# Performance work log

Measured on AMD Instinct MI355X. Metric: run time of the kernel, lower is better.

The kernel has to match this reference:

```python
import jax, jax.numpy as jnp
import numpy as np

D, H, DH, DF = 128, 8, 16, 512
N_Q, N_KV, E = 20000, 20000, 640000


def _xavier(key, shape):
    fan_in, fan_out = shape[1], shape[0]
    lim = float(np.sqrt(6.0 / (fan_in + fan_out)))
    return jax.random.uniform(key, shape, jnp.float32, -lim, lim)


def layer_norm(x, g, b, eps=1e-5):
    mu = jnp.mean(x, axis=-1, keepdims=True)
    var = jnp.var(x, axis=-1, keepdims=True)
    return (x - mu) * jax.lax.rsqrt(var + eps) * g + b


def setup_inputs() -> dict:
    key = jax.random.key(0)
    ks = jax.random.split(key, 12)
    return {
        "q_feat": jax.random.normal(ks[0], (N_Q, D), jnp.float32),
        "kv_feat": jax.random.normal(ks[1], (N_KV, D), jnp.float32),
        "src": jax.random.randint(ks[2], (E,), 0, N_KV, jnp.int32),
        "dst": jax.random.randint(ks[3], (E,), 0, N_Q, jnp.int32),
        "Wq": _xavier(ks[4], (H * DH, D)),
        "Wk": _xavier(ks[5], (H * DH, D)),
        "Wv": _xavier(ks[6], (H * DH, D)),
        "Wo": _xavier(ks[7], (D, H * DH)),
        "W1": _xavier(ks[8], (DF, D)),
        "bf1": jnp.zeros((DF,), jnp.float32),
        "W2": _xavier(ks[9], (D, DF)),
        "bf2": jnp.zeros((D,), jnp.float32),
        "ln1_g": jnp.ones((D,), jnp.float32),
        "ln1_b": jnp.zeros((D,), jnp.float32),
        "ln2_g": jnp.ones((D,), jnp.float32),
        "ln2_b": jnp.zeros((D,), jnp.float32),
    }


def reference(q_feat, kv_feat, src, dst, Wq, Wk, Wv, Wo, W1, bf1, W2, bf2,
              ln1_g, ln1_b, ln2_g, ln2_b):
    n_q = q_feat.shape[0]
    # projections -> [N, H, DH]
    q = (q_feat @ Wq.T).reshape(-1, H, DH)
    k = (kv_feat @ Wk.T).reshape(-1, H, DH)
    v = (kv_feat @ Wv.T).reshape(-1, H, DH)
    # edge scores: u_mul_v then sum over d_head, scaled (score per edge per head)
    score = jnp.einsum('ehd,ehd->eh', k[src], q[dst]) / np.sqrt(DH)
    # edge_softmax grouped by destination node
    mx = jax.ops.segment_max(score, dst, num_segments=n_q)  # [Nq, H]
    ex = jnp.exp(score - mx[dst])
    denom = jax.ops.segment_sum(ex, dst, num_segments=n_q)
    att = ex / denom[dst]  # [E, H]
    # weighted scatter-sum of values to destination nodes
    msg = v[src] * att[:, :, None]  # [E, H, DH]
    out = jax.ops.segment_sum(msg, dst, num_segments=n_q)  # [Nq, H, DH]
    sa = out.reshape(n_q, H * DH) @ Wo.T
    feat = layer_norm(q_feat + sa, ln1_g, ln1_b)
    ff = jax.nn.relu(feat @ W1.T + bf1) @ W2.T + bf2
    return layer_norm(feat + ff, ln2_g, ln2_b)
```

## Files before the change

### kernel.cpp

```cpp
#include <hip/hip_runtime.h>
#include <hip/hip_fp16.h>
#include <math.h>
#include <type_traits>

#define D 128
#define NH 8
#define DHD 16
#define DF 512
#define STR 128
#define NSH 8
#define SSL 64

typedef _Float16 half8 __attribute__((ext_vector_type(8)));
typedef _Float16 half4 __attribute__((ext_vector_type(4)));
typedef float f32x4 __attribute__((ext_vector_type(4)));


__global__ __launch_bounds__(256) void mega_kernel(
    const float* __restrict__ q_feat, const float* __restrict__ kv_feat,
    const float* __restrict__ Wq, const float* __restrict__ Wk,
    const float* __restrict__ Wv,
    __half* __restrict__ fq, __half* __restrict__ fkv, int NQ, int NKV,
    const int* __restrict__ dst, const int* __restrict__ src,
    int* __restrict__ cnt, unsigned short* __restrict__ srcg, int E,
    const float* __restrict__ Wo, const float* __restrict__ W1,
    const float* __restrict__ W2,
    __half* __restrict__ wo16, __half* __restrict__ w116, __half* __restrict__ w216) {
    __shared__ __align__(16) __half As[64 * 128];
    __shared__ __align__(16) __half Ws[64 * 128];

    int xt = blockIdx.x;
    int tid = threadIdx.x;

    if (xt >= 2) {
        if (xt == (int)gridDim.x - 1) {
            int g = blockIdx.y * 256 + tid;
            if (g < 36864) {
                const float* s;
                __half* d;
                int idx = g;
                if (idx < 4096) { s = Wo; d = wo16; }
                else if (idx < 20480) { idx -= 4096; s = W1; d = w116; }
                else { idx -= 20480; s = W2; d = w216; }
                float4 f = ((const float4*)s)[idx];
                ushort4 o;
                o.x = __half_as_ushort(__float2half(f.x));
                o.y = __half_as_ushort(__float2half(f.y));
                o.z = __half_as_ushort(__float2half(f.z));
                o.w = __half_as_ushort(__float2half(f.w));
                ((ushort4*)d)[idx] = o;
            }
            return;
        }
        int b = (xt - 2) * gridDim.y + blockIdx.y;
        int sh = (blockIdx.x + blockIdx.y * gridDim.x) & (NSH - 1);
        int i4 = b * 256 + tid;
        int base = i4 << 2;
        if (base < E) {
            if (base + 3 < E) {
                int4 d4 = ((const int4*)dst)[i4];
                int4 s4 = ((const int4*)src)[i4];
                int dd[4] = {d4.x, d4.y, d4.z, d4.w};
                int ss[4] = {s4.x, s4.y, s4.z, s4.w};
#pragma unroll
                for (int u = 0; u < 4; ++u) {
                    int p = atomicAdd(&cnt[dd[u] * NSH + sh], 1);
                    if (p < SSL)
                        srcg[((size_t)dd[u] << 9) + (sh << 6) + p] = (unsigned short)ss[u];
                }
            } else {
                for (int u = 0; u < 4 && base + u < E; ++u) {
                    int dn = dst[base + u];
                    int sn = src[base + u];
                    int p = atomicAdd(&cnt[dn * NSH + sh], 1);
                    if (p < SSL)
                        srcg[((size_t)dn << 9) + (sh << 6) + p] = (unsigned short)sn;
                }
            }
        }
        return;
    }

    const float* A = xt ? kv_feat : q_feat;
    __half* C = xt ? fkv : fq;
    int O = xt ? 256 : 128;
    int NCT = xt ? 4 : 2;
    int N = xt ? NKV : NQ;
    int row0 = blockIdx.y * 64;
    if (row0 >= N) return;

    int lane = tid & 63;
    int w = tid >> 6;
    int l16 = lane & 15, lq = lane >> 4;

#pragma unroll
    for (int i = 0; i < 4; ++i) {
        int f = tid + i * 256;
        int ln = f & 63;
        int mt = (f >> 6) & 3;
        int kc = f >> 8;
        int m = row0 + mt * 16 + (ln & 15);
        int k = kc * 32 + (ln >> 4) * 8;
        half8 v = {};
        if (m < N) {
            const float4* p = (const float4*)(A + (size_t)m * 128 + k);
            float4 f0 = p[0], f1 = p[1];
            v = (half8){(_Float16)f0.x, (_Float16)f0.y, (_Float16)f0.z, (_Float16)f0.w,
                        (_Float16)f1.x, (_Float16)f1.y, (_Float16)f1.z, (_Float16)f1.w};
        }
        ((half8*)As)[f] = v;
    }

    for (int ct = 0; ct < NCT; ++ct) {
        __syncthreads();
#pragma unroll
        for (int i = 0; i < 4; ++i) {
            int f = tid + i * 256;
            int ln = f & 63;
            int nt = (f >> 6) & 3;
            int kc = f >> 8;
            int n = ct * 64 + nt * 16 + (ln & 15);
            int k = kc * 32 + (ln >> 4) * 8;
            const float* Wsrc;
            int r;
            if (xt == 0) {
                Wsrc = Wq; r = n;
            } else {
                int h = n >> 5, qd = (n >> 3) & 3, isv = (n >> 2) & 1, d2 = n & 3;
                r = h * 16 + qd * 4 + d2;
                Wsrc = isv ? Wv : Wk;
            }
            const float4* p = (const float4*)(Wsrc + (size_t)r * 128 + k);
            float4 f0 = p[0], f1 = p[1];
            ((half8*)Ws)[f] = (half8){(_Float16)f0.x, (_Float16)f0.y, (_Float16)f0.z, (_Float16)f0.w,
                                      (_Float16)f1.x, (_Float16)f1.y, (_Float16)f1.z, (_Float16)f1.w};
        }
        __syncthreads();
        f32x4 acc[4];
#pragma unroll
        for (int j = 0; j < 4; ++j) acc[j] = (f32x4){0.f, 0.f, 0.f, 0.f};
#pragma unroll
        for (int kc = 0; kc < 4; ++kc) {
            half8 a = ((half8*)As)[(kc * 4 + w) * 64 + lane];
            half8 b[4];
#pragma unroll
            for (int j = 0; j < 4; ++j) b[j] = ((half8*)Ws)[(kc * 4 + j) * 64 + lane];
#pragma unroll
            for (int j = 0; j < 4; ++j)
                acc[j] = __builtin_amdgcn_mfma_f32_16x16x32_f16(a, b[j], acc[j], 0, 0, 0);
        }
#pragma unroll
        for (int j = 0; j < 4; ++j) {
            int c = ct * 64 + j * 16 + l16;
#pragma unroll
            for (int r = 0; r < 4; ++r) {
                int row = row0 + w * 16 + lq * 4 + r;
                if (row < N) C[(size_t)row * O + c] = __float2half(acc[j][r]);
            }
        }
    }
}


__global__ __launch_bounds__(256) void attn_kernel(
    const __half* __restrict__ q, const __half* __restrict__ kv,
    const unsigned short* __restrict__ srcg, const int* __restrict__ cnt,
    __half* __restrict__ out, int NQ) {
    __shared__ unsigned short list[4][STR];
    int wv = threadIdx.x >> 6;
    int n = blockIdx.x * 4 + wv;
    if (n >= NQ) return;
    int lane = threadIdx.x & 63;
    int eh = lane >> 5;
    int sub = lane & 31;
    int doff = sub << 2;

    const int4* c4 = (const int4*)(cnt + n * NSH);
    int4 ca = c4[0], cb = c4[1];
    int cs[8] = {ca.x, ca.y, ca.z, ca.w, cb.x, cb.y, cb.z, cb.w};
    int pre[9];
    pre[0] = 0;
#pragma unroll
    for (int r = 0; r < 8; ++r) {
        int cr = cs[r] < SSL ? cs[r] : SSL;
        pre[r + 1] = pre[r] + cr;
    }
    int total = pre[8] < STR ? pre[8] : STR;
    int sbase = n << 9;

    int i0 = 2 * lane, i1 = 2 * lane + 1;
    int sh0 = 0, of0 = i0, sh1 = 0, of1 = i1;
#pragma unroll
    for (int r = 0; r < 8; ++r) {
        if (i0 >= pre[r] && i0 < pre[r + 1]) { sh0 = r; of0 = i0 - pre[r]; }
        if (i1 >= pre[r] && i1 < pre[r + 1]) { sh1 = r; of1 = i1 - pre[r]; }
    }
    unsigned v0 = (i0 < total) ? (unsigned)srcg[sbase + (sh0 << 6) + of0] : 0xFFFFu;
    unsigned v1 = (i1 < total) ? (unsigned)srcg[sbase + (sh1 << 6) + of1] : 0xFFFFu;
#pragma unroll
    for (int k = 2; k <= 128; k <<= 1) {
#pragma unroll
        for (int j2 = k >> 1; j2 >= 2; j2 >>= 1) {
            int jl = j2 >> 1;
            bool asc = (lane & (k >> 1)) == 0;
            bool lowerhalf = (lane & jl) == 0;
            unsigned p0 = (unsigned)__shfl_xor((int)v0, jl);
            unsigned p1 = (unsigned)__shfl_xor((int)v1, jl);
            bool keepmin = (lowerhalf == asc);
            v0 = keepmin ? (v0 < p0 ? v0 : p0) : (v0 > p0 ? v0 : p0);
            v1 = keepmin ? (v1 < p1 ? v1 : p1) : (v1 > p1 ? v1 : p1);
        }
        {
            bool asc = (lane & (k >> 1)) == 0;
            unsigned lo = v0 < v1 ? v0 : v1, hi = v0 < v1 ? v1 : v0;
            v0 = asc ? lo : hi;
            v1 = asc ? hi : lo;
        }
    }
    list[wv][i0] = (unsigned short)v0;
    list[wv][i1] = (unsigned short)v1;

    half4 q4 = *(const half4*)(q + (size_t)n * D + doff);
    float q0 = (float)q4[0] * 0.25f, q1 = (float)q4[1] * 0.25f;
    float q2 = (float)q4[2] * 0.25f, q3 = (float)q4[3] * 0.25f;
    float lA = 0.f, lB = 0.f, lC = 0.f, lD = 0.f;
    f32x4 aA = {0.f, 0.f, 0.f, 0.f}, aB = {0.f, 0.f, 0.f, 0.f};
    f32x4 aC = {0.f, 0.f, 0.f, 0.f}, aD = {0.f, 0.f, 0.f, 0.f};
    int j = 0;
    for (; j + 8 <= total; j += 8) {
        int e0 = list[wv][j + eh];
        int e1 = list[wv][j + 2 + eh];
        int e2 = list[wv][j + 4 + eh];
        int e3 = list[wv][j + 6 + eh];
        half8 c0 = *(const half8*)(kv + (size_t)e0 * 256 + (sub << 3));
        half8 c1 = *(const half8*)(kv + (size_t)e1 * 256 + (sub << 3));
        half8 c2 = *(const half8*)(kv + (size_t)e2 * 256 + (sub << 3));
        half8 c3 = *(const half8*)(kv + (size_t)e3 * 256 + (sub << 3));
        float p0 = q0 * (float)c0[0] + q1 * (float)c0[1] + q2 * (float)c0[2] + q3 * (float)c0[3];
        float p1 = q0 * (float)c1[0] + q1 * (float)c1[1] + q2 * (float)c1[2] + q3 * (float)c1[3];
        float p2 = q0 * (float)c2[0] + q1 * (float)c2[1] + q2 * (float)c2[2] + q3 * (float)c2[3];
        float p3 = q0 * (float)c3[0] + q1 * (float)c3[1] + q2 * (float)c3[2] + q3 * (float)c3[3];
        p0 += __shfl_xor(p0, 1, 4); p0 += __shfl_xor(p0, 2, 4);
        p1 += __shfl_xor(p1, 1, 4); p1 += __shfl_xor(p1, 2, 4);
        p2 += __shfl_xor(p2, 1, 4); p2 += __shfl_xor(p2, 2, 4);
        p3 += __shfl_xor(p3, 1, 4); p3 += __shfl_xor(p3, 2, 4);
        float x0 = __expf(fminf(p0, 70.f));
        float x1 = __expf(fminf(p1, 70.f));
        float x2 = __expf(fminf(p2, 70.f));
        float x3 = __expf(fminf(p3, 70.f));
        lA += x0; lB += x1; lC += x2; lD += x3;
        aA[0] += x0 * (float)c0[4]; aA[1] += x0 * (float)c0[5];
        aA[2] += x0 * (float)c0[6]; aA[3] += x0 * (float)c0[7];
        aB[0] += x1 * (float)c1[4]; aB[1] += x1 * (float)c1[5];
        aB[2] += x1 * (float)c1[6]; aB[3] += x1 * (float)c1[7];
        aC[0] += x2 * (float)c2[4]; aC[1] += x2 * (float)c2[5];
        aC[2] += x2 * (float)c2[6]; aC[3] += x2 * (float)c2[7];
        aD[0] += x3 * (float)c3[4]; aD[1] += x3 * (float)c3[5];
        aD[2] += x3 * (float)c3[6]; aD[3] += x3 * (float)c3[7];
    }
    for (; j + 4 <= total; j += 4) {
        int e0 = list[wv][j + eh];
        int e1 = list[wv][j + 2 + eh];
        half8 c0 = *(const half8*)(kv + (size_t)e0 * 256 + (sub << 3));
        half8 c1 = *(const half8*)(kv + (size_t)e1 * 256 + (sub << 3));
        float p0 = q0 * (float)c0[0] + q1 * (float)c0[1] + q2 * (float)c0[2] + q3 * (float)c0[3];
        float p1 = q0 * (float)c1[0] + q1 * (float)c1[1] + q2 * (float)c1[2] + q3 * (float)c1[3];
        p0 += __shfl_xor(p0, 1, 4); p0 += __shfl_xor(p0, 2, 4);
        p1 += __shfl_xor(p1, 1, 4); p1 += __shfl_xor(p1, 2, 4);
        float x0 = __expf(fminf(p0, 70.f));
        float x1 = __expf(fminf(p1, 70.f));
        lA += x0; lB += x1;
        aA[0] += x0 * (float)c0[4]; aA[1] += x0 * (float)c0[5];
        aA[2] += x0 * (float)c0[6]; aA[3] += x0 * (float)c0[7];
        aB[0] += x1 * (float)c1[4]; aB[1] += x1 * (float)c1[5];
        aB[2] += x1 * (float)c1[6]; aB[3] += x1 * (float)c1[7];
    }
    for (; j < total; j += 2) {
        bool valid = (j + eh) < total;
        int e0 = list[wv][valid ? (j + eh) : 0];
        half8 c0 = *(const half8*)(kv + (size_t)e0 * 256 + (sub << 3));
        float p0 = q0 * (float)c0[0] + q1 * (float)c0[1] + q2 * (float)c0[2] + q3 * (float)c0[3];
        p0 += __shfl_xor(p0, 1, 4); p0 += __shfl_xor(p0, 2, 4);
        float x0 = valid ? __expf(fminf(p0, 70.f)) : 0.f;
        lA += x0;
        aA[0] += x0 * (float)c0[4]; aA[1] += x0 * (float)c0[5];
        aA[2] += x0 * (float)c0[6]; aA[3] += x0 * (float)c0[7];
    }
    float l = (lA + lB) + (lC + lD);
    f32x4 a;
#pragma unroll
    for (int i = 0; i < 4; ++i) a[i] = (aA[i] + aB[i]) + (aC[i] + aD[i]);
    l += __shfl_xor(l, 32);
#pragma unroll
    for (int i = 0; i < 4; ++i) a[i] += __shfl_xor(a[i], 32);
    if (eh == 0) {
        float rl = (l > 0.f) ? 1.f / l : 0.f;
        half4 o = {(_Float16)(a[0] * rl), (_Float16)(a[1] * rl),
                   (_Float16)(a[2] * rl), (_Float16)(a[3] * rl)};
        *(half4*)(out + (size_t)n * D + doff) = o;
    }
}


__device__ __forceinline__ int feat_idx64(int rr, int mt, int c) {
    return (((c >> 5) * 4 + mt) * 64 + ((c >> 3) & 3) * 16 + rr) * 8 + (c & 7);
}

__global__ __launch_bounds__(256) void tail_kernel(
    const __half* __restrict__ A , const __half* __restrict__ Wo16,
    const float* __restrict__ res1 ,
    const float* __restrict__ g1, const float* __restrict__ b1,
    const __half* __restrict__ W1h, const float* __restrict__ fb1,
    const __half* __restrict__ W2h, const float* __restrict__ fb2,
    const float* __restrict__ g2, const float* __restrict__ b2,
    float* __restrict__ out, int N) {
    __shared__ __align__(16) __half Feat[64 * 128];
    __shared__ __align__(16) __half S1[64 * 128];
    __shared__ __align__(16) __half S2[128 * 64];
    __shared__ __align__(16) __half Hs[64 * 64];
    int tid = threadIdx.x, lane = tid & 63, w = tid >> 6;
    int row0 = blockIdx.x * 64;
    int l16 = lane & 15, lq = lane >> 4;

#pragma unroll
    for (int i = 0; i < 4; ++i) {
        int f = tid + i * 256;
        int ln = f & 63, mt = (f >> 6) & 3, kc = f >> 8;
        int m = row0 + mt * 16 + (ln & 15);
        int k = kc * 32 + (ln >> 4) * 8;
        half8 av = {};
        if (m < N) av = *(const half8*)(A + (size_t)m * D + k);
        ((half8*)S1)[f] = av;
    }
    half8 rW[8];
#pragma unroll
    for (int i = 0; i < 8; ++i) {
        int f = tid + (i & 3) * 256;
        int kt = i >> 2;
        int ln = f & 63, ot = (f >> 6) & 7, kc2 = f >> 9;
        int o = ot * 16 + (ln & 15);
        int k = kt * 64 + kc2 * 32 + (ln >> 4) * 8;
        rW[i] = *(const half8*)(Wo16 + (size_t)o * D + k);
    }

    half8 r1[4], r2[4];
    auto ldw = [&](int hcx) {
#pragma unroll
        for (int i = 0; i < 4; ++i) {
            int f = tid + i * 256;
            int ln = f & 63, nt = (f >> 6) & 3, kc = f >> 8;
            int n = hcx * 64 + nt * 16 + (ln & 15);
            int k = kc * 32 + (ln >> 4) * 8;
            r1[i] = *(const half8*)(W1h + (size_t)n * D + k);
        }
#pragma unroll
        for (int i = 0; i < 4; ++i) {
            int f = tid + i * 256;
            int ln = f & 63, ot = (f >> 6) & 7, kc2 = f >> 9;
            int o = ot * 16 + (ln & 15);
            int k = hcx * 64 + kc2 * 32 + (ln >> 4) * 8;
            r2[i] = *(const half8*)(W2h + (size_t)o * DF + k);
        }
    };

    f32x4 acc[8];
#pragma unroll
    for (int j = 0; j < 8; ++j) acc[j] = (f32x4){0.f, 0.f, 0.f, 0.f};
#pragma unroll
    for (int kt = 0; kt < 2; ++kt) {
        __syncthreads();
#pragma unroll
        for (int i = 0; i < 4; ++i) ((half8*)S2)[tid + i * 256] = rW[kt * 4 + i];
        if (kt == 1) ldw(0);
        __syncthreads();
#pragma unroll
        for (int kc2 = 0; kc2 < 2; ++kc2) {
            half8 a = ((half8*)S1)[((kt * 2 + kc2) * 4 + w) * 64 + lane];
            half8 bf[8];
#pragma unroll
            for (int j = 0; j < 8; ++j) bf[j] = ((half8*)S2)[(kc2 * 8 + j) * 64 + lane];
#pragma unroll
            for (int j = 0; j < 8; ++j)
                acc[j] = __builtin_amdgcn_mfma_f32_16x16x32_f16(a, bf[j], acc[j], 0, 0, 0);
        }
    }
    __syncthreads();

#pragma unroll
    for (int r = 0; r < 4; ++r) {
        int rr = lq * 4 + r;
        int row = row0 + w * 16 + rr;
        bool valid = row < N;
        float vals[8];
        float s = 0.f, sq = 0.f;
#pragma unroll
        for (int j = 0; j < 8; ++j) {
            int c = j * 16 + l16;
            float v = acc[j][r];
            if (valid) v += res1[(size_t)row * D + c];
            vals[j] = v;
            s += v;
            sq += v * v;
        }
#pragma unroll
        for (int m = 1; m < 16; m <<= 1) {
            s += __shfl_xor(s, m, 16);
            sq += __shfl_xor(sq, m, 16);
        }
        float mu = s * (1.f / 128.f);
        float var = sq * (1.f / 128.f) - mu * mu;
        float inv = rsqrtf(var + 1e-5f);
#pragma unroll
        for (int j = 0; j < 8; ++j) {
            int c = j * 16 + l16;
            float o = (vals[j] - mu) * inv * g1[c] + b1[c];
            Feat[feat_idx64(rr, w, c)] = __float2half(o);
        }
    }
    __syncthreads();

    half8 a_all[4];
#pragma unroll
    for (int kc = 0; kc < 4; ++kc)
        a_all[kc] = ((half8*)Feat)[(kc * 4 + w) * 64 + lane];

    f32x4 oacc[8];
#pragma unroll
    for (int j = 0; j < 8; ++j) oacc[j] = (f32x4){0.f, 0.f, 0.f, 0.f};

    for (int hc = 0; hc < 8; ++hc) {
        __syncthreads();
#pragma unroll
        for (int i = 0; i < 4; ++i) ((half8*)S1)[tid + i * 256] = r1[i];
#pragma unroll
        for (int i = 0; i < 4; ++i) ((half8*)S2)[tid + i * 256] = r2[i];
        if (hc < 7) ldw(hc + 1);
        __syncthreads();
        f32x4 hacc[4];
#pragma unroll
        for (int j = 0; j < 4; ++j) hacc[j] = (f32x4){0.f, 0.f, 0.f, 0.f};
#pragma unroll
        for (int kc = 0; kc < 4; ++kc) {
            half8 b[4];
#pragma unroll
            for (int j = 0; j < 4; ++j) b[j] = ((half8*)S1)[(kc * 4 + j) * 64 + lane];
#pragma unroll
            for (int j = 0; j < 4; ++j)
                hacc[j] = __builtin_amdgcn_mfma_f32_16x16x32_f16(a_all[kc], b[j], hacc[j], 0, 0, 0);
        }
#pragma unroll
        for (int j = 0; j < 4; ++j) {
            float bias1 = fb1[hc * 64 + j * 16 + l16];
#pragma unroll
            for (int r = 0; r < 4; ++r) {
                float v = fmaxf(hacc[j][r] + bias1, 0.f);
                int kc2 = j >> 1;
                int lanep = ((j & 1) * 2 + (l16 >> 3)) * 16 + lq * 4 + r;
                Hs[((kc2 * 4 + w) * 64 + lanep) * 8 + (l16 & 7)] = __float2half(v);
            }
        }
        __syncthreads();
#pragma unroll
        for (int kc2 = 0; kc2 < 2; ++kc2) {
            half8 a = ((half8*)Hs)[(kc2 * 4 + w) * 64 + lane];
            half8 b[8];
#pragma unroll
            for (int ot = 0; ot < 8; ++ot) b[ot] = ((half8*)S2)[(kc2 * 8 + ot) * 64 + lane];
#pragma unroll
            for (int ot = 0; ot < 8; ++ot)
                oacc[ot] = __builtin_amdgcn_mfma_f32_16x16x32_f16(a, b[ot], oacc[ot], 0, 0, 0);
        }
    }

#pragma unroll
    for (int r = 0; r < 4; ++r) {
        int rr = lq * 4 + r;
        int row = row0 + w * 16 + rr;
        bool valid = row < N;
        float vals[8];
        float s = 0.f, sq = 0.f;
#pragma unroll
        for (int j = 0; j < 8; ++j) {
            int c = j * 16 + l16;
            float v = oacc[j][r] + fb2[c] + __half2float(Feat[feat_idx64(rr, w, c)]);
            vals[j] = v;
            s += v;
            sq += v * v;
        }
#pragma unroll
        for (int m = 1; m < 16; m <<= 1) {
            s += __shfl_xor(s, m, 16);
            sq += __shfl_xor(sq, m, 16);
        }
        float mu = s * (1.f / 128.f);
        float var = sq * (1.f / 128.f) - mu * mu;
        float inv = rsqrtf(var + 1e-5f);
        if (valid) {
#pragma unroll
            for (int j = 0; j < 8; ++j) {
                int c = j * 16 + l16;
                out[(size_t)row * D + c] = (vals[j] - mu) * inv * g2[c] + b2[c];
            }
        }
    }
}


extern "C" void kernel_launch(void* const* d_in, const int* in_sizes, int n_in,
                              void* d_out, int out_size, void* d_ws, size_t ws_size,
                              hipStream_t stream) {
    const float* q_feat = (const float*)d_in[0];
    const float* kv_feat = (const float*)d_in[1];
    const int* src = (const int*)d_in[2];
    const int* dst = (const int*)d_in[3];
    const float* Wq = (const float*)d_in[4];
    const float* Wk = (const float*)d_in[5];
    const float* Wv = (const float*)d_in[6];
    const float* Wo = (const float*)d_in[7];
    const float* W1 = (const float*)d_in[8];
    const float* bf1 = (const float*)d_in[9];
    const float* W2 = (const float*)d_in[10];
    const float* bf2 = (const float*)d_in[11];
    const float* ln1g = (const float*)d_in[12];
    const float* ln1b = (const float*)d_in[13];
    const float* ln2g = (const float*)d_in[14];
    const float* ln2b = (const float*)d_in[15];

    int NQ = in_sizes[0] / D;
    int NKV = in_sizes[1] / D;
    int E = in_sizes[2];
    float* out = (float*)d_out;

    char* base = (char*)d_ws;
    size_t off = 0;
    auto alloc = [&](size_t bytes) -> void* {
        void* p = base + off;
        off += (bytes + 255) & ~(size_t)255;
        return p;
    };
    __half* fq16 = (__half*)alloc((size_t)NQ * D * 2);
    __half* fkv = (__half*)alloc((size_t)NKV * 256 * 2);
    __half* fattn16 = (__half*)alloc((size_t)NQ * D * 2);
    int* cnt = (int*)alloc((size_t)NQ * NSH * 4);
    unsigned short* srcg = (unsigned short*)alloc((size_t)NQ * NSH * SSL * 2);
    __half* wo16 = (__half*)alloc((size_t)D * D * 2);
    __half* w116 = (__half*)alloc((size_t)DF * D * 2);
    __half* w216 = (__half*)alloc((size_t)D * DF * 2);

    hipMemsetAsync(cnt, 0, (size_t)NQ * NSH * sizeof(int), stream);

    dim3 blk(256);
    int NMX = NQ > NKV ? NQ : NKV;
    int ytiles = (NMX + 63) / 64;
    int fillBlocks = (E + 1023) / 1024;
    int fillPlanes = (fillBlocks + ytiles - 1) / ytiles;
    mega_kernel<<<dim3(3 + fillPlanes, ytiles), blk, 0, stream>>>(
        q_feat, kv_feat, Wq, Wk, Wv, fq16, fkv, NQ, NKV,
        dst, src, cnt, srcg, E, Wo, W1, W2, wo16, w116, w216);

    attn_kernel<<<(NQ + 3) / 4, blk, 0, stream>>>(fq16, fkv, srcg, cnt, fattn16, NQ);

    tail_kernel<<<(NQ + 63) / 64, blk, 0, stream>>>(
        fattn16, wo16, q_feat, ln1g, ln1b, w116, bf1, w216, bf2, ln2g, ln2b, out, NQ);
}
```

Baseline: 211.2 us.

## Shrink tail kernel LDS footprint and prefetch residuals to raise occupancy

Merges the Feat and Hs shared buffers into one FH buffer, cutting LDS per block from 64KB to 48KB, and sets launch bounds to allow 3 blocks per CU. Both Wo halves are staged into S1/S2 at once, which removes one barrier round in the first GEMM. The residual res1 values and the first W1/W2 chunk are loaded into registers early, overlapping their latency with the first GEMM. The LN1 output is kept in registers (fres) for the second residual instead of being reread from LDS. The extra registers may cause spills under the 3-block occupancy cap.

```diff
diff --git a/kernel.cpp b/kernel.cpp
--- a/kernel.cpp
+++ b/kernel.cpp
@@ -306,7 +306,7 @@
     return (((c >> 5) * 4 + mt) * 64 + ((c >> 3) & 3) * 16 + rr) * 8 + (c & 7);
 }
 
-__global__ __launch_bounds__(256) void tail_kernel(
+__global__ __launch_bounds__(256, 3) void tail_kernel(
     const __half* __restrict__ A , const __half* __restrict__ Wo16,
     const float* __restrict__ res1 ,
     const float* __restrict__ g1, const float* __restrict__ b1,
@@ -314,14 +314,14 @@
     const __half* __restrict__ W2h, const float* __restrict__ fb2,
     const float* __restrict__ g2, const float* __restrict__ b2,
     float* __restrict__ out, int N) {
-    __shared__ __align__(16) __half Feat[64 * 128];
     __shared__ __align__(16) __half S1[64 * 128];
     __shared__ __align__(16) __half S2[128 * 64];
-    __shared__ __align__(16) __half Hs[64 * 64];
+    __shared__ __align__(16) __half FH[64 * 128];
     int tid = threadIdx.x, lane = tid & 63, w = tid >> 6;
     int row0 = blockIdx.x * 64;
     int l16 = lane & 15, lq = lane >> 4;
 
+    half8 rA[4], rW[8];
 #pragma unroll
     for (int i = 0; i < 4; ++i) {
         int f = tid + i * 256;
@@ -330,9 +330,8 @@
         int k = kc * 32 + (ln >> 4) * 8;
         half8 av = {};
         if (m < N) av = *(const half8*)(A + (size_t)m * D + k);
-        ((half8*)S1)[f] = av;
-    }
-    half8 rW[8];
+        rA[i] = av;
+    }
 #pragma unroll
     for (int i = 0; i < 8; ++i) {
         int f = tid + (i & 3) * 256;
@@ -342,6 +341,13 @@
         int k = kt * 64 + kc2 * 32 + (ln >> 4) * 8;
         rW[i] = *(const half8*)(Wo16 + (size_t)o * D + k);
     }
+#pragma unroll
+    for (int i = 0; i < 4; ++i) ((half8*)FH)[tid + i * 256] = rA[i];
+#pragma unroll
+    for (int i = 0; i < 4; ++i) ((half8*)S1)[tid + i * 256] = rW[i];
+#pragma unroll
+    for (int i = 0; i < 4; ++i) ((half8*)S2)[tid + i * 256] = rW[4 + i];
+    __syncthreads();
 
     half8 r1[4], r2[4];
     auto ldw = [&](int hcx) {
@@ -362,29 +368,117 @@
             r2[i] = *(const half8*)(W2h + (size_t)o * DF + k);
         }
     };
+    ldw(0);
+    float rres[4][8];
+#pragma unroll
+    for (int r = 0; r < 4; ++r) {
+        int row = row0 + w * 16 + lq * 4 + r;
+        bool valid = row < N;
+#pragma unroll
+        for (int j = 0; j < 8; ++j)
+            rres[r][j] = valid ? res1[(size_t)row * D + j * 16 + l16] : 0.f;
+    }
 
     f32x4 acc[8];
 #pragma unroll
     for (int j = 0; j < 8; ++j) acc[j] = (f32x4){0.f, 0.f, 0.f, 0.f};
 #pragma unroll
-    for (int kt = 0; kt < 2; ++kt) {
+    for (int kc = 0; kc < 4; ++kc) {
+        half8 a = ((half8*)FH)[(kc * 4 + w) * 64 + lane];
+        const __half* Sx = (kc < 2) ? S1 : S2;
+        int kc2 = kc & 1;
+        half8 bf[8];
+#pragma unroll
+        for (int j = 0; j < 8; ++j) bf[j] = ((half8*)Sx)[(kc2 * 8 + j) * 64 + lane];
+#pragma unroll
+        for (int j = 0; j < 8; ++j)
+            acc[j] = __builtin_amdgcn_mfma_f32_16x16x32_f16(a, bf[j], acc[j], 0, 0, 0);
+    }
+    __syncthreads();
+
+    half8 fres[4];
+#pragma unroll
+    for (int r = 0; r < 4; ++r) {
+        int rr = lq * 4 + r;
+        float vals[8];
+        float s = 0.f, sq = 0.f;
+#pragma unroll
+        for (int j = 0; j < 8; ++j) {
+            float v = acc[j][r] + rres[r][j];
+            vals[j] = v;
+            s += v;
+            sq += v * v;
+        }
+#pragma unroll
+        for (int m = 1; m < 16; m <<= 1) {
+            s += __shfl_xor(s, m, 16);
+            sq += __shfl_xor(sq, m, 16);
+        }
+        float mu = s * (1.f / 128.f);
+        float var = sq * (1.f / 128.f) - mu * mu;
+        float inv = rsqrtf(var + 1e-5f);
+#pragma unroll
+        for (int j = 0; j < 8; ++j) {
+            int c = j * 16 + l16;
+            float o = (vals[j] - mu) * inv * g1[c] + b1[c];
+            FH[feat_idx64(rr, w, c)] = __float2half(o);
+            fres[r][j] = (_Float16)o;
+        }
+    }
+    __syncthreads();
+
+    half8 a_all[4];
+#pragma unroll
+    for (int kc = 0; kc < 4; ++kc)
+        a_all[kc] = ((half8*)FH)[(kc * 4 + w) * 64 + lane];
+
+    f32x4 oacc[8];
+#pragma unroll
+    for (int j = 0; j < 8; ++j) oacc[j] = (f32x4){0.f, 0.f, 0.f, 0.f};
+
+    for (int hc = 0; hc < 8; ++hc) {
         __syncthreads();
 #pragma unroll
-        for (int i = 0; i < 4; ++i) ((half8*)S2)[tid + i * 256] = rW[kt * 4 + i];
-        if (kt == 1) ldw(0);
+        for (int i = 0; i < 4; ++i) ((half8*)S1)[tid + i * 256] = r1[i];
+#pragma unroll
+        for (int i = 0; i < 4; ++i) ((half8*)S2)[tid + i * 256] = r2[i];
+        if (hc < 7) ldw(hc + 1);
         __syncthreads();
+        f32x4 hacc[4];
+#pragma unroll
+        for (int j = 0; j < 4; ++j) hacc[j] = (f32x4){0.f, 0.f, 0.f, 0.f};
+#pragma unroll
+        for (int kc = 0; kc < 4; ++kc) {
+            half8 b[4];
+#pragma unroll
+            for (int j = 0; j < 4; ++j) b[j] = ((half8*)S1)[(kc * 4 + j) * 64 + lane];
+#pragma unroll
+            for (int j = 0; j < 4; ++j)
+                hacc[j] = __builtin_amdgcn_mfma_f32_16x16x32_f16(a_all[kc], b[j], hacc[j], 0, 0, 0);
+        }
+#pragma unroll
+        for (int j = 0; j < 4; ++j) {
+            float bias1 = fb1[hc * 64 + j * 16 + l16];
+#pragma unroll
+            for (int r = 0; r < 4; ++r) {
+                float v = fmaxf(hacc[j][r] + bias1, 0.f);
+                int kc2 = j >> 1;
+                int lanep = ((j & 1) * 2 + (l16 >> 3)) * 16 + lq * 4 + r;
+                FH[((kc2 * 4 + w) * 64 + lanep) * 8 + (l16 & 7)] = __float2half(v);
+            }
+        }
+        __syncthreads();
 #pragma unroll
         for (int kc2 = 0; kc2 < 2; ++kc2) {
-            half8 a = ((half8*)S1)[((kt * 2 + kc2) * 4 + w) * 64 + lane];
-            half8 bf[8];
-#pragma unroll
-            for (int j = 0; j < 8; ++j) bf[j] = ((half8*)S2)[(kc2 * 8 + j) * 64 + lane];
-#pragma unroll
-            for (int j = 0; j < 8; ++j)
-                acc[j] = __builtin_amdgcn_mfma_f32_16x16x32_f16(a, bf[j], acc[j], 0, 0, 0);
-        }
-    }
-    __syncthreads();
+            half8 a = ((half8*)FH)[(kc2 * 4 + w) * 64 + lane];
+            half8 b[8];
+#pragma unroll
+            for (int ot = 0; ot < 8; ++ot) b[ot] = ((half8*)S2)[(kc2 * 8 + ot) * 64 + lane];
+#pragma unroll
+            for (int ot = 0; ot < 8; ++ot)
+                oacc[ot] = __builtin_amdgcn_mfma_f32_16x16x32_f16(a, b[ot], oacc[ot], 0, 0, 0);
+        }
+    }
 
 #pragma unroll
     for (int r = 0; r < 4; ++r) {
@@ -396,93 +490,7 @@
 #pragma unroll
         for (int j = 0; j < 8; ++j) {
             int c = j * 16 + l16;
-            float v = acc[j][r];
-            if (valid) v += res1[(size_t)row * D + c];
-            vals[j] = v;
-            s += v;
-            sq += v * v;
-        }
-#pragma unroll
-        for (int m = 1; m < 16; m <<= 1) {
-            s += __shfl_xor(s, m, 16);
-            sq += __shfl_xor(sq, m, 16);
-        }
-        float mu = s * (1.f / 128.f);
-        float var = sq * (1.f / 128.f) - mu * mu;
-        float inv = rsqrtf(var + 1e-5f);
-#pragma unroll
-        for (int j = 0; j < 8; ++j) {
-            int c = j * 16 + l16;
-            float o = (vals[j] - mu) * inv * g1[c] + b1[c];
-            Feat[feat_idx64(rr, w, c)] = __float2half(o);
-        }
-    }
-    __syncthreads();
-
-    half8 a_all[4];
-#pragma unroll
-    for (int kc = 0; kc < 4; ++kc)
-        a_all[kc] = ((half8*)Feat)[(kc * 4 + w) * 64 + lane];
-
-    f32x4 oacc[8];
-#pragma unroll
-    for (int j = 0; j < 8; ++j) oacc[j] = (f32x4){0.f, 0.f, 0.f, 0.f};
-
-    for (int hc = 0; hc < 8; ++hc) {
-        __syncthreads();
-#pragma unroll
-        for (int i = 0; i < 4; ++i) ((half8*)S1)[tid + i * 256] = r1[i];
-#pragma unroll
-        for (int i = 0; i < 4; ++i) ((half8*)S2)[tid + i * 256] = r2[i];
-        if (hc < 7) ldw(hc + 1);
-        __syncthreads();
-        f32x4 hacc[4];
-#pragma unroll
-        for (int j = 0; j < 4; ++j) hacc[j] = (f32x4){0.f, 0.f, 0.f, 0.f};
-#pragma unroll
-        for (int kc = 0; kc < 4; ++kc) {
-            half8 b[4];
-#pragma unroll
-            for (int j = 0; j < 4; ++j) b[j] = ((half8*)S1)[(kc * 4 + j) * 64 + lane];
-#pragma unroll
-            for (int j = 0; j < 4; ++j)
-                hacc[j] = __builtin_amdgcn_mfma_f32_16x16x32_f16(a_all[kc], b[j], hacc[j], 0, 0, 0);
-        }
-#pragma unroll
-        for (int j = 0; j < 4; ++j) {
-            float bias1 = fb1[hc * 64 + j * 16 + l16];
-#pragma unroll
-            for (int r = 0; r < 4; ++r) {
-                float v = fmaxf(hacc[j][r] + bias1, 0.f);
-                int kc2 = j >> 1;
-                int lanep = ((j & 1) * 2 + (l16 >> 3)) * 16 + lq * 4 + r;
-                Hs[((kc2 * 4 + w) * 64 + lanep) * 8 + (l16 & 7)] = __float2half(v);
-            }
-        }
-        __syncthreads();
-#pragma unroll
-        for (int kc2 = 0; kc2 < 2; ++kc2) {
-            half8 a = ((half8*)Hs)[(kc2 * 4 + w) * 64 + lane];
-            half8 b[8];
-#pragma unroll
-            for (int ot = 0; ot < 8; ++ot) b[ot] = ((half8*)S2)[(kc2 * 8 + ot) * 64 + lane];
-#pragma unroll
-            for (int ot = 0; ot < 8; ++ot)
-                oacc[ot] = __builtin_amdgcn_mfma_f32_16x16x32_f16(a, b[ot], oacc[ot], 0, 0, 0);
-        }
-    }
-
-#pragma unroll
-    for (int r = 0; r < 4; ++r) {
-        int rr = lq * 4 + r;
-        int row = row0 + w * 16 + rr;
-        bool valid = row < N;
-        float vals[8];
-        float s = 0.f, sq = 0.f;
-#pragma unroll
-        for (int j = 0; j < 8; ++j) {
-            int c = j * 16 + l16;
-            float v = oacc[j][r] + fb2[c] + __half2float(Feat[feat_idx64(rr, w, c)]);
+            float v = oacc[j][r] + fb2[c] + (float)fres[r][j];
             vals[j] = v;
             s += v;
             sq += v * v;
```

After: 208.4 us. Within noise of the previous version (-1.3%).
